# Performance work log

Measured on AMD Instinct MI355X. Metric: run time of the kernel, lower is better.

## Reference

```python
import jax, jax.numpy as jnp
import numpy as np

B, T, E, H, D = 2, 1024, 2048, 16, 64
DEPTH = 12
LAMBDA_INIT = 0.8 - 0.6 * float(np.exp(-0.3 * DEPTH))
EPS = 1e-5


def _rope_interleaved(x):
    # x: (b, t, heads, d), rotate interleaved even/odd pairs
    d = x.shape[-1]
    inv_freq = 1.0 / (10000.0 ** (jnp.arange(0, d, 2, dtype=jnp.float32) / d))  # (d/2,)
    ang = jnp.arange(x.shape[1], dtype=jnp.float32)[:, None] * inv_freq[None, :]  # (t, d/2)
    cos = jnp.cos(ang)[None, :, None, :].astype(x.dtype)
    sin = jnp.sin(ang)[None, :, None, :].astype(x.dtype)
    x1, x2 = x[..., 0::2], x[..., 1::2]
    r1 = x1 * cos - x2 * sin
    r2 = x1 * sin + x2 * cos
    return jnp.stack([r1, r2], axis=-1).reshape(x.shape)


def setup_inputs() -> dict:
    key = jax.random.key(0)
    ks = jax.random.split(key, 11)
    w_scale = 0.02
    return {
        "x": jax.random.normal(ks[0], (B, T, E), jnp.float32),
        "rel_pos": jax.random.uniform(ks[1], (T, D), jnp.float32),
        "wq": jax.random.normal(ks[2], (E, E), jnp.float32) * w_scale,
        "wk": jax.random.normal(ks[3], (E, E), jnp.float32) * w_scale,
        "wv": jax.random.normal(ks[4], (E, E), jnp.float32) * w_scale,
        "lambda_q1": jax.random.normal(ks[5], (D,), jnp.float32) * 0.1,
        "lambda_q2": jax.random.normal(ks[6], (D,), jnp.float32) * 0.1,
        "lambda_k1": jax.random.normal(ks[7], (D,), jnp.float32) * 0.1,
        "lambda_k2": jax.random.normal(ks[8], (D,), jnp.float32) * 0.1,
        "subln_w": jnp.ones((2 * D,), jnp.float32),
        "wo": jax.random.normal(ks[9], (E, E), jnp.float32) * w_scale,
    }


def reference(x, rel_pos, wq, wk, wv, lambda_q1, lambda_q2, lambda_k1, lambda_k2, subln_w, wo):
    b, t, e = x.shape
    scaling = D ** 0.5
    # projections; q,k have 2*H heads of dim D, v has H heads of dim 2*D
    q = (x @ wq.T).reshape(b, t, 2 * H, D)
    k = (x @ wk.T).reshape(b, t, 2 * H, D)
    v = (x @ wv.T).reshape(b, t, H, 2 * D)
    k = k * rel_pos[None, :, None, :]
    q = _rope_interleaved(q)
    k = _rope_interleaved(k)
    q = q.transpose(0, 2, 1, 3)  # (b, 2H, t, D)
    k = k.transpose(0, 2, 1, 3)
    v = v.transpose(0, 2, 1, 3)  # (b, H, t, 2D)
    scores = jnp.einsum("bhqd,bhkd->bhqk", q, k) / scaling
    causal = jnp.tril(jnp.ones((t, t), bool))
    scores = jnp.where(causal[None, None], scores, jnp.float32(-1e9))
    p = jax.nn.softmax(scores.astype(jnp.float32), axis=-1).astype(x.dtype)
    lam1 = jnp.exp(jnp.sum(lambda_q1 * lambda_k1))
    lam2 = jnp.exp(jnp.sum(lambda_q2 * lambda_k2))
    lam_full = lam1 - lam2 + LAMBDA_INIT
    p = p.reshape(b, H, 2, t, t)
    pw = p[:, :, 0] - lam_full * p[:, :, 1]  # (b, H, t, t)
    attn = jnp.einsum("bhqk,bhkd->bhqd", pw, v)  # (b, H, t, 2D)
    # RMSNorm over last dim (2D)
    ms = jnp.mean(attn.astype(jnp.float32) ** 2, axis=-1, keepdims=True)
    attn = (attn * jax.lax.rsqrt(ms + EPS)).astype(x.dtype) * subln_w
    out = attn.transpose(0, 2, 1, 3).reshape(b, t, H * 2 * D) @ wo.T
    return out
```

## Files before the change

kernel.cpp:

```cpp
#include <hip/hip_runtime.h>

typedef __bf16 bf16x8 __attribute__((ext_vector_type(8)));
typedef float f32x4 __attribute__((ext_vector_type(4)));

__device__ __forceinline__ float bf2f(unsigned short u) {
  return __uint_as_float(((unsigned)u) << 16);
}
__device__ __forceinline__ unsigned short f2bf(float f) {
  unsigned u = __float_as_uint(f);
  return (unsigned short)((u + 0x7fffu + ((u >> 16) & 1u)) >> 16);
}
__device__ __forceinline__ unsigned pack2(float a, float b) {
  return (unsigned)f2bf(a) | ((unsigned)f2bf(b) << 16);
}

#define SWZB(row, byte) ((byte) ^ (((row) & 7) << 4))

#define AS_GLOBAL(p) ((const __attribute__((address_space(1))) void*)(p))
#define AS_LDS(p) ((__attribute__((address_space(3))) void*)(p))

__global__ __launch_bounds__(256) void pre_kernel(
    const float* __restrict__ s0, const float* __restrict__ s1,
    const float* __restrict__ s2, const float* __restrict__ s3,
    unsigned short* __restrict__ d0, unsigned short* __restrict__ d1,
    unsigned short* __restrict__ d2, unsigned short* __restrict__ d3,
    const float* __restrict__ lq1, const float* __restrict__ lq2,
    const float* __restrict__ lk1, const float* __restrict__ lk2,
    float* __restrict__ lamb, int n4) {
  if (blockIdx.y == 4) {
    if (blockIdx.x == 0 && threadIdx.x < 64) {
      int l = threadIdx.x;
      float p1 = lq1[l] * lk1[l];
      float p2 = lq2[l] * lk2[l];
      #pragma unroll
      for (int off = 32; off; off >>= 1) {
        p1 += __shfl_xor(p1, off);
        p2 += __shfl_xor(p2, off);
      }
      if (l == 0) lamb[0] = expf(p1) - expf(p2) + 0.7836057665316245f;
    }
    return;
  }
  int idx = blockIdx.x * 256 + threadIdx.x;
  if (idx >= n4) return;
  const float* s;
  unsigned short* d;
  switch (blockIdx.y) {
    case 0: s = s0; d = d0; break;
    case 1: s = s1; d = d1; break;
    case 2: s = s2; d = d2; break;
    default: s = s3; d = d3; break;
  }
  float4 v = reinterpret_cast<const float4*>(s)[idx];
  uint2 pk;
  pk.x = pack2(v.x, v.y);
  pk.y = pack2(v.z, v.w);
  reinterpret_cast<uint2*>(d)[idx] = pk;
}

template <typename OT>
__global__ __launch_bounds__(256)
void gemm_bk64(const unsigned short* __restrict__ A, const unsigned short* __restrict__ Bw,
               OT* __restrict__ C, int M, int K, int ldc) {
  __shared__ __align__(16) unsigned short As[128 * 64];
  __shared__ __align__(16) unsigned short Bs[128 * 64];
  const int tid = threadIdx.x;
  const int bm = blockIdx.x * 128, bn = blockIdx.y * 128;
  const int lane = tid & 63, wave = tid >> 6;
  const int wm = (wave >> 1) * 64, wn = (wave & 1) * 64;
  const int rr = lane & 15, lg = lane >> 4;
  const int srow = lane >> 3;
  const int sblk = (lane & 7) ^ srow;
  const char* ab = reinterpret_cast<const char*>(As);
  const char* bb = reinterpret_cast<const char*>(Bs);
  OT* Cb = C + (size_t)(bn / ldc) * ((size_t)M * ldc) + (bn % ldc);
  f32x4 acc[4][4] = {};
  for (int kt = 0; kt < K; kt += 64) {
    __syncthreads();
    #pragma unroll
    for (int j = 0; j < 4; ++j) {
      int s = wave + j * 4;
      const unsigned short* asrc = &A[(long)(bm + s * 8 + srow) * K + kt + sblk * 8];
      __builtin_amdgcn_global_load_lds(AS_GLOBAL(asrc), AS_LDS(&As[s * 512]), 16, 0, 0);
      const unsigned short* bsrc = &Bw[(long)(bn + s * 8 + srow) * K + kt + sblk * 8];
      __builtin_amdgcn_global_load_lds(AS_GLOBAL(bsrc), AS_LDS(&Bs[s * 512]), 16, 0, 0);
    }
    __syncthreads();
    bf16x8 af[4][2], bq[4][2];
    #pragma unroll
    for (int i = 0; i < 4; ++i) {
      int row = wm + i * 16 + rr;
      af[i][0] = *reinterpret_cast<const bf16x8*>(ab + row * 128 + SWZB(row, lg * 16));
      af[i][1] = *reinterpret_cast<const bf16x8*>(ab + row * 128 + SWZB(row, 64 + lg * 16));
    }
    #pragma unroll
    for (int j = 0; j < 4; ++j) {
      int row = wn + j * 16 + rr;
      bq[j][0] = *reinterpret_cast<const bf16x8*>(bb + row * 128 + SWZB(row, lg * 16));
      bq[j][1] = *reinterpret_cast<const bf16x8*>(bb + row * 128 + SWZB(row, 64 + lg * 16));
    }
    #pragma unroll
    for (int i = 0; i < 4; ++i)
      #pragma unroll
      for (int j = 0; j < 4; ++j) {
        acc[i][j] = __builtin_amdgcn_mfma_f32_16x16x32_bf16(af[i][0], bq[j][0], acc[i][j], 0, 0, 0);
        acc[i][j] = __builtin_amdgcn_mfma_f32_16x16x32_bf16(af[i][1], bq[j][1], acc[i][j], 0, 0, 0);
      }
  }
  const int cc = lane & 15;
  #pragma unroll
  for (int i = 0; i < 4; ++i)
    #pragma unroll
    for (int j = 0; j < 4; ++j)
      #pragma unroll
      for (int r = 0; r < 4; ++r) {
        long row = bm + wm + i * 16 + lg * 4 + r;
        long col = wn + j * 16 + cc;
        float v = acc[i][j][r];
        if constexpr (sizeof(OT) == 2) Cb[row * ldc + col] = f2bf(v);
        else                           Cb[row * ldc + col] = v;
      }
}

#define ROPE_BLKS 8192
#define CVT_BLKS 4096
#define TRN_BLKS 1024
__global__ __launch_bounds__(256) void mid_kernel(
    const unsigned short* __restrict__ qraw, const unsigned short* __restrict__ kraw,
    const unsigned short* __restrict__ vraw, const float* __restrict__ rel,
    const float* __restrict__ wo,
    unsigned short* __restrict__ qatt, unsigned short* __restrict__ katt,
    unsigned short* __restrict__ wob, unsigned short* __restrict__ vtb) {
  __shared__ unsigned short ls[64][68];
  const int bid = blockIdx.x;
  const int tid = threadIdx.x;
  if (bid < 2 * ROPE_BLKS) {
    const int use_rel = bid >= ROPE_BLKS;
    const unsigned short* raw = use_rel ? kraw : qraw;
    unsigned short* outp = use_rel ? katt : qatt;
    int idx = (bid & (ROPE_BLKS - 1)) * 256 + tid;
    int i = idx & 31;
    int t = (idx >> 5) & 1023;
    int hp = (idx >> 15) & 31;
    int b = idx >> 20;
    int src = (b * 1024 + t) * 2048 + hp * 64 + 2 * i;
    unsigned pair = *reinterpret_cast<const unsigned*>(&raw[src]);
    float x1 = __uint_as_float(pair << 16);
    float x2 = __uint_as_float(pair & 0xffff0000u);
    if (use_rel) {
      x1 *= rel[t * 64 + 2 * i];
      x2 *= rel[t * 64 + 2 * i + 1];
    }
    float inv = expf(-0.28782313662425574f * (float)i);
    float s, c;
    sincosf((float)t * inv, &s, &c);
    int dst = ((b * 32 + hp) * 1024 + t) * 64 + 2 * i;
    *reinterpret_cast<unsigned*>(&outp[dst]) = pack2(x1 * c - x2 * s, x1 * s + x2 * c);
  } else if (bid < 2 * ROPE_BLKS + CVT_BLKS) {
    int idx = (bid - 2 * ROPE_BLKS) * 256 + tid;
    float4 v = reinterpret_cast<const float4*>(wo)[idx];
    uint2 pk;
    pk.x = pack2(v.x, v.y);
    pk.y = pack2(v.z, v.w);
    reinterpret_cast<uint2*>(wob)[idx] = pk;
  } else {
    int tb = bid - (2 * ROPE_BLKS + CVT_BLKS);
    const int t0 = (tb & 15) * 64, n0 = ((tb >> 4) & 31) * 64, b = tb >> 9;
    #pragma unroll
    for (int p = 0; p < 4; ++p) {
      int idx = p * 256 + tid;
      int tl = idx >> 4, nq = (idx & 15) * 4;
      *reinterpret_cast<uint2*>(&ls[tl][nq]) = *reinterpret_cast<const uint2*>(
          &vraw[((long)(b * 1024 + t0 + tl)) * 2048 + n0 + nq]);
    }
    __syncthreads();
    #pragma unroll
    for (int p = 0; p < 4; ++p) {
      int idx = p * 256 + tid;
      int nl = idx >> 4, tq = (idx & 15) * 4;
      uint2 o;
      o.x = (unsigned)ls[tq + 0][nl] | ((unsigned)ls[tq + 1][nl] << 16);
      o.y = (unsigned)ls[tq + 2][nl] | ((unsigned)ls[tq + 3][nl] << 16);
      *reinterpret_cast<uint2*>(&vtb[((long)(b * 2048 + n0 + nl)) * 1024 + t0 + tq]) = o;
    }
  }
}

__global__ __launch_bounds__(256) void attn_mfma(
    const unsigned short* __restrict__ Qa,
    const unsigned short* __restrict__ Ka,
    const unsigned short* __restrict__ Vt,
    const float* __restrict__ lam_p,
    const float* __restrict__ subln,
    unsigned short* __restrict__ O) {
  const int n = blockIdx.x;
  const int c = n & 7, m = n >> 3;
  const int g = c * 4 + (m >> 4);
  const int bx = m & 15;
  const int h = g & 15, b = g >> 4;

  const int tid = threadIdx.x;
  const int lane = tid & 63, w = tid >> 6;
  const int lg = lane >> 4, cc = lane & 15;
  const int hh = w >> 1, qoff = (w & 1) * 16;

  __shared__ __align__(16) unsigned short KsBuf[2][2 * 64 * 64];
  __shared__ __align__(16) unsigned short VsBuf[2][128 * 64];
  __shared__ __align__(16) unsigned short PbBuf[4 * 16 * 64];

  const float lam = lam_p[0];
  char* ksb0 = reinterpret_cast<char*>(&KsBuf[0][0]);
  char* vsb0 = reinterpret_cast<char*>(&VsBuf[0][0]);
  char* pbb = reinterpret_cast<char*>(PbBuf) + w * 2048;
  float* cb = reinterpret_cast<float*>(&KsBuf[0][0]);

  const int srow = lane >> 3;
  const int sblk = (lane & 7) ^ srow;
  auto STAGE = [&](char* kd, char* vd, int k0) {
    #pragma unroll
    for (int j = 0; j < 4; ++j) {
      int s = w * 4 + j;
      int sh = s >> 3, rg = s & 7;
      const unsigned short* ksrc =
          &Ka[(((long)(b * 32 + 2 * h + sh)) * 1024 + k0 + rg * 8 + srow) * 64 + sblk * 8];
      __builtin_amdgcn_global_load_lds(AS_GLOBAL(ksrc), AS_LDS(kd + sh * 8192 + rg * 1024),
                                       16, 0, 0);
      const unsigned short* vsrc =
          &Vt[((long)(b * 2048 + h * 128 + s * 8 + srow)) * 1024 + k0 + sblk * 8];
      __builtin_amdgcn_global_load_lds(AS_GLOBAL(vsrc), AS_LDS(vd + s * 1024), 16, 0, 0);
    }
  };

  float sl[8];
  #pragma unroll
  for (int jc = 0; jc < 8; ++jc) sl[jc] = subln[jc * 16 + cc];

  const long kbase = (long)((b * 32 + 2 * h + hh) * 1024);

  for (int pass = 0; pass < 2; ++pass) {
    const int q0 = (pass ? (31 - bx) : bx) * 32;
    const int nt = ((q0 + 31) >> 6) + 1;

    __syncthreads();
    STAGE(ksb0, vsb0, 0);

    bf16x8 qf[2];
    {
      const long qrow = q0 + qoff + cc;
      #pragma unroll
      for (int c2 = 0; c2 < 2; ++c2)
        qf[c2] = *reinterpret_cast<const bf16x8*>(&Qa[(kbase + qrow) * 64 + c2 * 32 + lg * 8]);
    }
    f32x4 acc_o[8];
    float mS[4], lS[4];
    #pragma unroll
    for (int jc = 0; jc < 8; ++jc) acc_o[jc] = (f32x4){0.f, 0.f, 0.f, 0.f};
    #pragma unroll
    for (int r = 0; r < 4; ++r) { mS[r] = -1e30f; lS[r] = 0.f; }

    __syncthreads();

    int cur = 0;
    for (int tile = 0; tile < nt; ++tile) {
      if (tile + 1 < nt)
        STAGE(ksb0 + (cur ^ 1) * 16384, vsb0 + (cur ^ 1) * 16384, (tile + 1) * 64);
      char* kb = ksb0 + cur * 16384;
      char* vb = vsb0 + cur * 16384;

      const int k0 = tile * 64;
      f32x4 s4[4];
      #pragma unroll
      for (int j = 0; j < 4; ++j) s4[j] = (f32x4){0.f, 0.f, 0.f, 0.f};
      #pragma unroll
      for (int j = 0; j < 4; ++j) {
        int row = j * 16 + cc;
        const char* base = kb + hh * 8192 + row * 128;
        bf16x8 kb0 = *reinterpret_cast<const bf16x8*>(base + SWZB(row, lg * 16));
        bf16x8 kb1 = *reinterpret_cast<const bf16x8*>(base + SWZB(row, lg * 16 + 64));
        s4[j] = __builtin_amdgcn_mfma_f32_16x16x32_bf16(qf[0], kb0, s4[j], 0, 0, 0);
        s4[j] = __builtin_amdgcn_mfma_f32_16x16x32_bf16(qf[1], kb1, s4[j], 0, 0, 0);
      }
      #pragma unroll
      for (int j = 0; j < 4; ++j) {
        int kcol = k0 + j * 16 + cc;
        #pragma unroll
        for (int r = 0; r < 4; ++r) {
          int qrow = q0 + qoff + lg * 4 + r;
          float s = s4[j][r] * 0.125f;
          s4[j][r] = (kcol > qrow) ? -1e30f : s;
        }
      }
      float rescv[4];
      #pragma unroll
      for (int r = 0; r < 4; ++r) {
        float mx = fmaxf(fmaxf(s4[0][r], s4[1][r]), fmaxf(s4[2][r], s4[3][r]));
        mx = fmaxf(mx, __shfl_xor(mx, 1));
        mx = fmaxf(mx, __shfl_xor(mx, 2));
        mx = fmaxf(mx, __shfl_xor(mx, 4));
        mx = fmaxf(mx, __shfl_xor(mx, 8));
        float mold = mS[r];
        float mnew = fmaxf(mold, mx);
        mS[r] = mnew;
        float rsc = __expf(mold - mnew);
        rescv[r] = rsc;
        float ls = 0.f;
        #pragma unroll
        for (int j = 0; j < 4; ++j) {
          float p = __expf(s4[j][r] - mnew);
          s4[j][r] = p;
          ls += p;
        }
        ls += __shfl_xor(ls, 1);
        ls += __shfl_xor(ls, 2);
        ls += __shfl_xor(ls, 4);
        ls += __shfl_xor(ls, 8);
        lS[r] = lS[r] * rsc + ls;
      }
      #pragma unroll
      for (int j = 0; j < 4; ++j)
        #pragma unroll
        for (int r = 0; r < 4; ++r) {
          int rowl = lg * 4 + r;
          *reinterpret_cast<unsigned short*>(
              pbb + rowl * 128 + SWZB(rowl, (j * 16 + cc) * 2)) = f2bf(s4[j][r]);
        }

      bf16x8 pa[2];
      #pragma unroll
      for (int c2 = 0; c2 < 2; ++c2)
        pa[c2] = *reinterpret_cast<const bf16x8*>(pbb + cc * 128 + SWZB(cc, lg * 16 + c2 * 64));
      #pragma unroll
      for (int jc = 0; jc < 8; ++jc)
        #pragma unroll
        for (int r = 0; r < 4; ++r)
          acc_o[jc][r] *= rescv[r];
      #pragma unroll
      for (int jc = 0; jc < 8; ++jc) {
        int row = jc * 16 + cc;
        const char* base = vb + row * 128;
        bf16x8 vf0 = *reinterpret_cast<const bf16x8*>(base + SWZB(row, lg * 16));
        bf16x8 vf1 = *reinterpret_cast<const bf16x8*>(base + SWZB(row, lg * 16 + 64));
        acc_o[jc] = __builtin_amdgcn_mfma_f32_16x16x32_bf16(pa[0], vf0, acc_o[jc], 0, 0, 0);
        acc_o[jc] = __builtin_amdgcn_mfma_f32_16x16x32_bf16(pa[1], vf1, acc_o[jc], 0, 0, 0);
      }

      __syncthreads();
      cur ^= 1;
    }

    if (hh == 1) {
      #pragma unroll
      for (int r = 0; r < 4; ++r) {
        float inv2 = lam / lS[r];
        int row = qoff + lg * 4 + r;
        #pragma unroll
        for (int jc = 0; jc < 8; ++jc)
          cb[row * 128 + ((jc ^ (row & 7)) * 16 + cc)] = acc_o[jc][r] * inv2;
      }
    }
    __syncthreads();
    if (hh == 0) {
      float sc[4];
      #pragma unroll
      for (int r = 0; r < 4; ++r) {
        float inv1 = 1.f / lS[r];
        int row = qoff + lg * 4 + r;
        float ss = 0.f;
        #pragma unroll
        for (int jc = 0; jc < 8; ++jc) {
          float at = acc_o[jc][r] * inv1 - cb[row * 128 + ((jc ^ (row & 7)) * 16 + cc)];
          acc_o[jc][r] = at;
          ss += at * at;
        }
        ss += __shfl_xor(ss, 1);
        ss += __shfl_xor(ss, 2);
        ss += __shfl_xor(ss, 4);
        ss += __shfl_xor(ss, 8);
        sc[r] = rsqrtf(ss * (1.f / 128.f) + 1e-5f);
      }
      #pragma unroll
      for (int r = 0; r < 4; ++r) {
        long qrow = q0 + qoff + lg * 4 + r;
        #pragma unroll
        for (int jc = 0; jc < 8; ++jc) {
          O[(long)(b * 1024 + qrow) * 2048 + h * 128 + jc * 16 + cc] =
              f2bf(acc_o[jc][r] * sc[r] * sl[jc]);
        }
      }
    }
  }
}

extern "C" void kernel_launch(void* const* d_in, const int* in_sizes, int n_in,
                              void* d_out, int out_size, void* d_ws, size_t ws_size,
                              hipStream_t stream) {
  (void)in_sizes; (void)n_in; (void)out_size; (void)ws_size;
  const float* x    = (const float*)d_in[0];
  const float* rel  = (const float*)d_in[1];
  const float* wq   = (const float*)d_in[2];
  const float* wk   = (const float*)d_in[3];
  const float* wv   = (const float*)d_in[4];
  const float* lq1  = (const float*)d_in[5];
  const float* lq2  = (const float*)d_in[6];
  const float* lk1  = (const float*)d_in[7];
  const float* lk2  = (const float*)d_in[8];
  const float* subw = (const float*)d_in[9];
  const float* wo   = (const float*)d_in[10];
  float* out = (float*)d_out;

  char* ws = (char*)d_ws;
  const size_t SZ = (size_t)2048 * 2048 * 2;
  unsigned short* wqkvb = (unsigned short*)(ws);
  unsigned short* vtb   = (unsigned short*)(ws);
  unsigned short* qatt  = (unsigned short*)(ws + SZ);
  unsigned short* katt  = (unsigned short*)(ws + 2 * SZ);
  unsigned short* xbf   = (unsigned short*)(ws + 3 * SZ);
  unsigned short* wob   = xbf;
  unsigned short* qraw  = (unsigned short*)(ws + 4 * SZ);
  unsigned short* kraw  = (unsigned short*)(ws + 5 * SZ);
  unsigned short* vraw  = (unsigned short*)(ws + 6 * SZ);
  unsigned short* aout  = qraw;
  float* lamb           = (float*)(ws + 7 * SZ);

  const int N4 = 2048 * 2048 / 4;
  pre_kernel<<<dim3(N4 / 256, 5), 256, 0, stream>>>(
      x, wq, wk, wv, xbf, wqkvb, wqkvb + (size_t)2048 * 2048,
      wqkvb + (size_t)2 * 2048 * 2048, lq1, lq2, lk1, lk2, lamb, N4);

  gemm_bk64<unsigned short><<<dim3(16, 48), 256, 0, stream>>>(xbf, wqkvb, qraw,
                                                              2048, 2048, 2048);

  mid_kernel<<<2 * ROPE_BLKS + CVT_BLKS + TRN_BLKS, 256, 0, stream>>>(
      qraw, kraw, vraw, rel, wo, qatt, katt, wob, vtb);

  attn_mfma<<<dim3(512), 256, 0, stream>>>(qatt, katt, vtb, lamb, subw, aout);

  gemm_bk64<float><<<dim3(16, 16), 256, 0, stream>>>(aout, wob, out, 2048, 2048, 2048);
}
```

Measured before the change: 191.1 us.

## Replace double-buffered K/V staging with single buffer to raise occupancy

Drops the ping-pong LDS buffers for K and V tiles in the attention kernel and stages each tile synchronously, with barriers before and after the load. Halving LDS per block, together with launch_bounds(256,4), is meant to fit more blocks per CU so that other waves hide the load latency instead of in-kernel prefetch. The cost is that global-to-LDS loads are no longer overlapped with MFMA work inside a block, and there are extra barriers per tile.

```diff
diff --git a/kernel.cpp b/kernel.cpp
--- a/kernel.cpp
+++ b/kernel.cpp
@@ -186,7 +186,7 @@
   }
 }
 
-__global__ __launch_bounds__(256) void attn_mfma(
+__global__ __launch_bounds__(256, 4) void attn_mfma(
     const unsigned short* __restrict__ Qa,
     const unsigned short* __restrict__ Ka,
     const unsigned short* __restrict__ Vt,
@@ -204,30 +204,30 @@
   const int lg = lane >> 4, cc = lane & 15;
   const int hh = w >> 1, qoff = (w & 1) * 16;
 
-  __shared__ __align__(16) unsigned short KsBuf[2][2 * 64 * 64];
-  __shared__ __align__(16) unsigned short VsBuf[2][128 * 64];
+  __shared__ __align__(16) unsigned short KsBuf[2 * 64 * 64];
+  __shared__ __align__(16) unsigned short VsBuf[128 * 64];
   __shared__ __align__(16) unsigned short PbBuf[4 * 16 * 64];
 
   const float lam = lam_p[0];
-  char* ksb0 = reinterpret_cast<char*>(&KsBuf[0][0]);
-  char* vsb0 = reinterpret_cast<char*>(&VsBuf[0][0]);
+  char* ksb = reinterpret_cast<char*>(&KsBuf[0]);
+  char* vsb = reinterpret_cast<char*>(&VsBuf[0]);
   char* pbb = reinterpret_cast<char*>(PbBuf) + w * 2048;
-  float* cb = reinterpret_cast<float*>(&KsBuf[0][0]);
+  float* cb = reinterpret_cast<float*>(&KsBuf[0]);
 
   const int srow = lane >> 3;
   const int sblk = (lane & 7) ^ srow;
-  auto STAGE = [&](char* kd, char* vd, int k0) {
+  auto STAGE = [&](int k0) {
     #pragma unroll
     for (int j = 0; j < 4; ++j) {
       int s = w * 4 + j;
       int sh = s >> 3, rg = s & 7;
       const unsigned short* ksrc =
           &Ka[(((long)(b * 32 + 2 * h + sh)) * 1024 + k0 + rg * 8 + srow) * 64 + sblk * 8];
-      __builtin_amdgcn_global_load_lds(AS_GLOBAL(ksrc), AS_LDS(kd + sh * 8192 + rg * 1024),
+      __builtin_amdgcn_global_load_lds(AS_GLOBAL(ksrc), AS_LDS(ksb + sh * 8192 + rg * 1024),
                                        16, 0, 0);
       const unsigned short* vsrc =
           &Vt[((long)(b * 2048 + h * 128 + s * 8 + srow)) * 1024 + k0 + sblk * 8];
-      __builtin_amdgcn_global_load_lds(AS_GLOBAL(vsrc), AS_LDS(vd + s * 1024), 16, 0, 0);
+      __builtin_amdgcn_global_load_lds(AS_GLOBAL(vsrc), AS_LDS(vsb + s * 1024), 16, 0, 0);
     }
   };
 
@@ -241,9 +241,6 @@
     const int q0 = (pass ? (31 - bx) : bx) * 32;
     const int nt = ((q0 + 31) >> 6) + 1;
 
-    __syncthreads();
-    STAGE(ksb0, vsb0, 0);
-
     bf16x8 qf[2];
     {
       const long qrow = q0 + qoff + cc;
@@ -258,23 +255,19 @@
     #pragma unroll
     for (int r = 0; r < 4; ++r) { mS[r] = -1e30f; lS[r] = 0.f; }
 
-    __syncthreads();
-
-    int cur = 0;
     for (int tile = 0; tile < nt; ++tile) {
-      if (tile + 1 < nt)
-        STAGE(ksb0 + (cur ^ 1) * 16384, vsb0 + (cur ^ 1) * 16384, (tile + 1) * 64);
-      char* kb = ksb0 + cur * 16384;
-      char* vb = vsb0 + cur * 16384;
-
       const int k0 = tile * 64;
+      __syncthreads();
+      STAGE(k0);
+      __syncthreads();
+
       f32x4 s4[4];
       #pragma unroll
       for (int j = 0; j < 4; ++j) s4[j] = (f32x4){0.f, 0.f, 0.f, 0.f};
       #pragma unroll
       for (int j = 0; j < 4; ++j) {
         int row = j * 16 + cc;
-        const char* base = kb + hh * 8192 + row * 128;
+        const char* base = ksb + hh * 8192 + row * 128;
         bf16x8 kb0 = *reinterpret_cast<const bf16x8*>(base + SWZB(row, lg * 16));
         bf16x8 kb1 = *reinterpret_cast<const bf16x8*>(base + SWZB(row, lg * 16 + 64));
         s4[j] = __builtin_amdgcn_mfma_f32_16x16x32_bf16(qf[0], kb0, s4[j], 0, 0, 0);
@@ -337,17 +330,15 @@
       #pragma unroll
       for (int jc = 0; jc < 8; ++jc) {
         int row = jc * 16 + cc;
-        const char* base = vb + row * 128;
+        const char* base = vsb + row * 128;
         bf16x8 vf0 = *reinterpret_cast<const bf16x8*>(base + SWZB(row, lg * 16));
         bf16x8 vf1 = *reinterpret_cast<const bf16x8*>(base + SWZB(row, lg * 16 + 64));
         acc_o[jc] = __builtin_amdgcn_mfma_f32_16x16x32_bf16(pa[0], vf0, acc_o[jc], 0, 0, 0);
         acc_o[jc] = __builtin_amdgcn_mfma_f32_16x16x32_bf16(pa[1], vf1, acc_o[jc], 0, 0, 0);
       }
-
-      __syncthreads();
-      cur ^= 1;
-    }
-
+    }
+
+    __syncthreads();
     if (hh == 1) {
       #pragma unroll
       for (int r = 0; r < 4; ++r) {
@@ -388,6 +379,7 @@
         }
       }
     }
+    __syncthreads();
   }
 }
 
```

After: 222.6 us. 1.17x slower.
